# Kernel tuning notes

Hardware: AMD Instinct MI355X
Metric: run time of the kernel (lower is better)

The kernel has to match this reference:

```python
import jax, jax.numpy as jnp
import numpy as np


def setup_inputs() -> dict:
    key = jax.random.key(0)
    k1, k2, k3, k4 = jax.random.split(key, 4)
    B, n, f, k = 32768, 512, 30, 40
    X = jax.random.normal(k1, (B, n), dtype=jnp.float32)
    w1 = jax.random.normal(k2, (n, 1), dtype=jnp.float32) * 0.01
    b = jnp.zeros((1,), dtype=jnp.float32)
    v = jax.random.normal(k3, (n, f, k), dtype=jnp.float32) * 0.01
    feature2field = jax.random.randint(k4, (n,), 0, f, dtype=jnp.int32)
    return {"X": X, "w1": w1, "b": b, "v": v, "feature2field": feature2field}


def reference(X, w1, b, v, feature2field):
    # linear terms: [B]
    linear = (X @ w1).reshape(-1) + b[0]
    n = v.shape[0]
    # A[i, j] = v[i, feature2field[j]]  -> [n, n, k]
    A = v[:, feature2field, :]
    # pair coefficient C[i, j] = sum_k v[i, field[j], k] * v[j, field[i], k]
    C = jnp.einsum('ijk,jik->ij', A, A)
    # strict upper triangle matches the i<j loop in the original
    Cm = C * jnp.triu(jnp.ones((n, n), dtype=C.dtype), k=1)
    # interaction[b] = sum_{i<j} C[i,j] * X[b,i] * X[b,j]
    inter = jnp.einsum('bi,ij,bj->b', X, Cm, X)
    logits = linear + inter
    return jax.nn.sigmoid(logits)
```

## Files before the change

### kernel.cpp

```cpp
#include <hip/hip_runtime.h>
#include <hip/hip_bf16.h>
#include <math.h>


#define N_FEAT 512
#define FK 1200
#define KDIM 40
#define B_ROWS 32768
#define BM 64
#define BK 64

typedef __attribute__((ext_vector_type(8))) short short8;
typedef __attribute__((ext_vector_type(4))) float f32x4;

__device__ __forceinline__ unsigned short bf16_rne(float f) {
    union { float f; unsigned int u; } c; c.f = f;
    unsigned int u = c.u;
    u += 0x7fffu + ((u >> 16) & 1u);
    return (unsigned short)(u >> 16);
}

__device__ __forceinline__ float bf16_to_f(unsigned short h) {
    union { unsigned int u; float f; } c;
    c.u = ((unsigned int)h) << 16;
    return c.f;
}

__device__ __forceinline__ void async_copy16(const void* g, void* l) {
    __builtin_amdgcn_global_load_lds(
        (const __attribute__((address_space(1))) void*)g,
        (__attribute__((address_space(3))) void*)l,
        16, 0, 0);
}

__global__ __launch_bounds__(256) void build_w16(const float* __restrict__ v,
                                                 const int* __restrict__ f2f,
                                                 unsigned short* __restrict__ W16) {
    const int j = blockIdx.x * 256 + threadIdx.x;
    const int i = blockIdx.y;
    const int fi = f2f[i];
    const int fj = f2f[j];
    const float4* a = (const float4*)(v + (size_t)i * FK + (size_t)fj * KDIM);
    const float4* c = (const float4*)(v + (size_t)j * FK + (size_t)fi * KDIM);
    float acc = 0.f;
#pragma unroll
    for (int q = 0; q < KDIM / 4; ++q) {
        float4 av = a[q], cv = c[q];
        acc = fmaf(av.x, cv.x, acc);
        acc = fmaf(av.y, cv.y, acc);
        acc = fmaf(av.z, cv.z, acc);
        acc = fmaf(av.w, cv.w, acc);
    }
    W16[(size_t)i * N_FEAT + j] = (i == j) ? (unsigned short)0 : bf16_rne(0.5f * acc);
}

__global__ __launch_bounds__(256, 2) void ffm_fused(const float* __restrict__ X,
                                                    const unsigned short* __restrict__ W16,
                                                    const float* __restrict__ w1,
                                                    const float* __restrict__ bvec,
                                                    float* __restrict__ out) {
    __shared__ __align__(16) unsigned short As[BM * N_FEAT];
    __shared__ __align__(16) unsigned short Bs[128 * BK];
    float* part = (float*)Bs;

    const int tid  = threadIdx.x;
    const int lane = tid & 63;
    const int wave = tid >> 6;
    const int wm = wave & 1;
    const int wn = wave >> 1;
    const int quad = lane >> 4;
    const int l16  = lane & 15;

    const size_t row0 = (size_t)blockIdx.x * BM;

    {
        const float4* X4 = (const float4*)(X + row0 * N_FEAT);
        for (int u = 0; u < 16; ++u) {
            const int g  = u * 256 + tid;
            const int r  = g >> 6;
            const int cc = g & 63;
            float4 f0 = X4[r * 128 + cc * 2];
            float4 f1 = X4[r * 128 + cc * 2 + 1];
            union { unsigned short us[8]; short8 v; } pk;
            pk.us[0] = bf16_rne(f0.x);
            pk.us[1] = bf16_rne(f0.y);
            pk.us[2] = bf16_rne(f0.z);
            pk.us[3] = bf16_rne(f0.w);
            pk.us[4] = bf16_rne(f1.x);
            pk.us[5] = bf16_rne(f1.y);
            pk.us[6] = bf16_rne(f1.z);
            pk.us[7] = bf16_rne(f1.w);
            *(short8*)(As + r * N_FEAT + ((cc ^ (r & 7)) << 3)) = pk.v;
        }
    }

    const int srow = lane >> 3;
    const int scol = (((lane & 7) ^ srow) << 3);
    const int aswz = l16 & 7;

    float rs[2][4];
#pragma unroll
    for (int mi = 0; mi < 2; ++mi)
#pragma unroll
        for (int reg = 0; reg < 4; ++reg) rs[mi][reg] = 0.f;

    for (int cb = 0; cb < 4; ++cb) {
        const int col0 = cb * 128;

        f32x4 acc[2][4];
#pragma unroll
        for (int mi = 0; mi < 2; ++mi)
#pragma unroll
            for (int ni = 0; ni < 4; ++ni)
                acc[mi][ni] = (f32x4){0.f, 0.f, 0.f, 0.f};

        for (int k0 = 0; k0 < N_FEAT; k0 += BK) {
            __syncthreads();
#pragma unroll
            for (int c = 0; c < 4; ++c) {
                const int chunk = wave * 4 + c;
                const int r = chunk * 8 + srow;
                async_copy16(W16 + (size_t)(col0 + r) * N_FEAT + k0 + scol,
                             Bs + chunk * 512);
            }
            __syncthreads();

#pragma unroll
            for (int kk = 0; kk < 2; ++kk) {
                short8 a[2], b[4];
                const int kc = (k0 >> 3) + kk * 4 + quad;
#pragma unroll
                for (int mi = 0; mi < 2; ++mi) {
                    const int ar = wm * 32 + mi * 16 + l16;
                    a[mi] = *(const short8*)(As + ar * N_FEAT + ((kc ^ aswz) << 3));
                }
                const int swc = ((kk * 4 + quad) ^ aswz) << 3;
#pragma unroll
                for (int ni = 0; ni < 4; ++ni) {
                    const int br = wn * 64 + ni * 16 + l16;
                    b[ni] = *(const short8*)(Bs + br * BK + swc);
                }
#pragma unroll
                for (int mi = 0; mi < 2; ++mi)
#pragma unroll
                    for (int ni = 0; ni < 4; ++ni)
                        acc[mi][ni] = __builtin_amdgcn_mfma_f32_16x16x32_bf16(
                            a[mi], b[ni], acc[mi][ni], 0, 0, 0);
            }
        }

        float w1v[4];
#pragma unroll
        for (int ni = 0; ni < 4; ++ni)
            w1v[ni] = w1[col0 + wn * 64 + ni * 16 + l16];
#pragma unroll
        for (int mi = 0; mi < 2; ++mi) {
#pragma unroll
            for (int ni = 0; ni < 4; ++ni) {
                const int gc = col0 + wn * 64 + ni * 16 + l16;
#pragma unroll
                for (int reg = 0; reg < 4; ++reg) {
                    const int row = wm * 32 + mi * 16 + quad * 4 + reg;
                    const int adr = row * N_FEAT + ((((gc >> 3) ^ (row & 7)) << 3) | (gc & 7));
                    const float xf = bf16_to_f(As[adr]);
                    rs[mi][reg] = fmaf(xf, acc[mi][ni][reg] + w1v[ni], rs[mi][reg]);
                }
            }
        }
    }

    __syncthreads();

#pragma unroll
    for (int mi = 0; mi < 2; ++mi)
#pragma unroll
        for (int reg = 0; reg < 4; ++reg) {
            float r = rs[mi][reg];
#pragma unroll
            for (int off = 1; off < 16; off <<= 1)
                r += __shfl_xor(r, off, 16);
            if (l16 == 0)
                part[wn * BM + wm * 32 + mi * 16 + quad * 4 + reg] = r;
        }
    __syncthreads();

    if (tid < BM) {
        const float t = part[tid] + part[BM + tid] + bvec[0];
        out[row0 + tid] = 1.0f / (1.0f + expf(-t));
    }
}

extern "C" void kernel_launch(void* const* d_in, const int* in_sizes, int n_in,
                              void* d_out, int out_size, void* d_ws, size_t ws_size,
                              hipStream_t stream) {
    const float* X   = (const float*)d_in[0];
    const float* w1  = (const float*)d_in[1];
    const float* b   = (const float*)d_in[2];
    const float* v   = (const float*)d_in[3];
    const int*   f2f = (const int*)d_in[4];
    float* out = (float*)d_out;

    unsigned short* W16 = (unsigned short*)d_ws;

    build_w16<<<dim3(2, N_FEAT), 256, 0, stream>>>(v, f2f, W16);
    ffm_fused<<<B_ROWS / BM, 256, 0, stream>>>(X, W16, w1, b, out);
}
```

Before: 128.2 us.

## Load W fragments directly from global memory instead of staging through LDS

Removes the LDS staging buffer for the W16 tiles and the two barriers per K step. Each wave now loads its MFMA B fragments straight from global memory (L2-resident, 512x512 bf16) in a fully unrolled 16-step K loop. This drops synchronisation and LDS traffic. In exchange, every wave pair re-reads the same W rows from cache, and global latency is exposed with no explicit prefetch.

```diff
diff --git a/kernel.cpp b/kernel.cpp
--- a/kernel.cpp
+++ b/kernel.cpp
@@ -8,7 +8,6 @@
 #define KDIM 40
 #define B_ROWS 32768
 #define BM 64
-#define BK 64
 
 typedef __attribute__((ext_vector_type(8))) short short8;
 typedef __attribute__((ext_vector_type(4))) float f32x4;
@@ -24,13 +23,6 @@
     union { unsigned int u; float f; } c;
     c.u = ((unsigned int)h) << 16;
     return c.f;
-}
-
-__device__ __forceinline__ void async_copy16(const void* g, void* l) {
-    __builtin_amdgcn_global_load_lds(
-        (const __attribute__((address_space(1))) void*)g,
-        (__attribute__((address_space(3))) void*)l,
-        16, 0, 0);
 }
 
 __global__ __launch_bounds__(256) void build_w16(const float* __restrict__ v,
@@ -60,8 +52,7 @@
                                                     const float* __restrict__ bvec,
                                                     float* __restrict__ out) {
     __shared__ __align__(16) unsigned short As[BM * N_FEAT];
-    __shared__ __align__(16) unsigned short Bs[128 * BK];
-    float* part = (float*)Bs;
+    __shared__ float part[2 * BM];
 
     const int tid  = threadIdx.x;
     const int lane = tid & 63;
@@ -70,6 +61,7 @@
     const int wn = wave >> 1;
     const int quad = lane >> 4;
     const int l16  = lane & 15;
+    const int aswz = l16 & 7;
 
     const size_t row0 = (size_t)blockIdx.x * BM;
 
@@ -93,10 +85,7 @@
             *(short8*)(As + r * N_FEAT + ((cc ^ (r & 7)) << 3)) = pk.v;
         }
     }
-
-    const int srow = lane >> 3;
-    const int scol = (((lane & 7) ^ srow) << 3);
-    const int aswz = l16 & 7;
+    __syncthreads();
 
     float rs[2][4];
 #pragma unroll
@@ -114,39 +103,29 @@
             for (int ni = 0; ni < 4; ++ni)
                 acc[mi][ni] = (f32x4){0.f, 0.f, 0.f, 0.f};
 
-        for (int k0 = 0; k0 < N_FEAT; k0 += BK) {
-            __syncthreads();
+        const unsigned short* pb[4];
 #pragma unroll
-            for (int c = 0; c < 4; ++c) {
-                const int chunk = wave * 4 + c;
-                const int r = chunk * 8 + srow;
-                async_copy16(W16 + (size_t)(col0 + r) * N_FEAT + k0 + scol,
-                             Bs + chunk * 512);
-            }
-            __syncthreads();
+        for (int ni = 0; ni < 4; ++ni)
+            pb[ni] = W16 + (size_t)(col0 + wn * 64 + ni * 16 + l16) * N_FEAT + quad * 8;
 
 #pragma unroll
-            for (int kk = 0; kk < 2; ++kk) {
-                short8 a[2], b[4];
-                const int kc = (k0 >> 3) + kk * 4 + quad;
+        for (int kk = 0; kk < 16; ++kk) {
+            short8 a[2], b[4];
 #pragma unroll
-                for (int mi = 0; mi < 2; ++mi) {
-                    const int ar = wm * 32 + mi * 16 + l16;
-                    a[mi] = *(const short8*)(As + ar * N_FEAT + ((kc ^ aswz) << 3));
-                }
-                const int swc = ((kk * 4 + quad) ^ aswz) << 3;
+            for (int ni = 0; ni < 4; ++ni)
+                b[ni] = *(const short8*)(pb[ni] + kk * 32);
+            const int kc = kk * 4 + quad;
 #pragma unroll
-                for (int ni = 0; ni < 4; ++ni) {
-                    const int br = wn * 64 + ni * 16 + l16;
-                    b[ni] = *(const short8*)(Bs + br * BK + swc);
-                }
+            for (int mi = 0; mi < 2; ++mi) {
+                const int ar = wm * 32 + mi * 16 + l16;
+                a[mi] = *(const short8*)(As + ar * N_FEAT + ((kc ^ aswz) << 3));
+            }
 #pragma unroll
-                for (int mi = 0; mi < 2; ++mi)
+            for (int mi = 0; mi < 2; ++mi)
 #pragma unroll
-                    for (int ni = 0; ni < 4; ++ni)
-                        acc[mi][ni] = __builtin_amdgcn_mfma_f32_16x16x32_bf16(
-                            a[mi], b[ni], acc[mi][ni], 0, 0, 0);
-            }
+                for (int ni = 0; ni < 4; ++ni)
+                    acc[mi][ni] = __builtin_amdgcn_mfma_f32_16x16x32_bf16(
+                        a[mi], b[ni], acc[mi][ni], 0, 0, 0);
         }
 
         float w1v[4];
@@ -168,8 +147,6 @@
             }
         }
     }
-
-    __syncthreads();
 
 #pragma unroll
     for (int mi = 0; mi < 2; ++mi)
```

New measurement: 164.0 us. 27.9% more time.

## Double-buffer W tiles with async prefetch and use 8 waves per block

Applied to the files above, without the earlier changes.

Moves the fused FFM kernel from 256 to 512 threads, so each of 8 waves computes a 32x32 sub-tile instead of 32x64. W16 tiles are now double-buffered in LDS, and the next stage is prefetched with async global-to-LDS loads, synchronised by explicit vmcnt waits and raw barriers instead of two __syncthreads per k-step. The first W tile is issued before the X conversion, and w1 loads are hoisted out of the loop. The changes aim to hide global load latency and raise occupancy, at the cost of more LDS, more barriers per block and fragile manual waitcnt handling.

```diff
diff --git a/kernel.cpp b/kernel.cpp
--- a/kernel.cpp
+++ b/kernel.cpp
@@ -32,6 +32,8 @@
         (__attribute__((address_space(3))) void*)l,
         16, 0, 0);
 }
+
+#define FENCE() asm volatile("" ::: "memory")
 
 __global__ __launch_bounds__(256) void build_w16(const float* __restrict__ v,
                                                  const int* __restrict__ f2f,
@@ -54,14 +56,14 @@
     W16[(size_t)i * N_FEAT + j] = (i == j) ? (unsigned short)0 : bf16_rne(0.5f * acc);
 }
 
-__global__ __launch_bounds__(256, 2) void ffm_fused(const float* __restrict__ X,
+__global__ __launch_bounds__(512, 2) void ffm_fused(const float* __restrict__ X,
                                                     const unsigned short* __restrict__ W16,
                                                     const float* __restrict__ w1,
                                                     const float* __restrict__ bvec,
                                                     float* __restrict__ out) {
     __shared__ __align__(16) unsigned short As[BM * N_FEAT];
-    __shared__ __align__(16) unsigned short Bs[128 * BK];
-    float* part = (float*)Bs;
+    __shared__ __align__(16) unsigned short Bs[2][128 * BK];
+    __shared__ float part[4 * BM];
 
     const int tid  = threadIdx.x;
     const int lane = tid & 63;
@@ -70,13 +72,40 @@
     const int wn = wave >> 1;
     const int quad = lane >> 4;
     const int l16  = lane & 15;
+    const int aswz = l16 & 7;
 
     const size_t row0 = (size_t)blockIdx.x * BM;
 
+    const int srow = lane >> 3;
+    const int scol = (((lane & 7) ^ srow) << 3);
+
+    float w1v[4][2];
+#pragma unroll
+    for (int cb = 0; cb < 4; ++cb)
+#pragma unroll
+        for (int ni = 0; ni < 2; ++ni)
+            w1v[cb][ni] = w1[cb * 128 + wn * 32 + ni * 16 + l16];
+    const float bias = bvec[0];
+
+    auto stage = [&](int s) {
+        const int col0 = (s >> 3) * 128;
+        const int k0   = (s & 7) * 64;
+        unsigned short* dst = (unsigned short*)Bs[s & 1];
+#pragma unroll
+        for (int c = 0; c < 2; ++c) {
+            const int chunk = wave * 2 + c;
+            const int r = chunk * 8 + srow;
+            async_copy16(W16 + (size_t)(col0 + r) * N_FEAT + k0 + scol,
+                         dst + chunk * 512);
+        }
+    };
+
+    stage(0);
     {
         const float4* X4 = (const float4*)(X + row0 * N_FEAT);
-        for (int u = 0; u < 16; ++u) {
-            const int g  = u * 256 + tid;
+#pragma unroll
+        for (int u = 0; u < 8; ++u) {
+            const int g  = u * 512 + tid;
             const int r  = g >> 6;
             const int cc = g & 63;
             float4 f0 = X4[r * 128 + cc * 2];
@@ -93,10 +122,9 @@
             *(short8*)(As + r * N_FEAT + ((cc ^ (r & 7)) << 3)) = pk.v;
         }
     }
-
-    const int srow = lane >> 3;
-    const int scol = (((lane & 7) ^ srow) << 3);
-    const int aswz = l16 & 7;
+    asm volatile("s_waitcnt lgkmcnt(0)" ::: "memory");
+    __builtin_amdgcn_s_barrier();
+    FENCE();
 
     float rs[2][4];
 #pragma unroll
@@ -104,30 +132,33 @@
 #pragma unroll
         for (int reg = 0; reg < 4; ++reg) rs[mi][reg] = 0.f;
 
+    f32x4 acc[2][2];
+#pragma unroll
+    for (int mi = 0; mi < 2; ++mi)
+#pragma unroll
+        for (int ni = 0; ni < 2; ++ni)
+            acc[mi][ni] = (f32x4){0.f, 0.f, 0.f, 0.f};
+
+#pragma unroll
     for (int cb = 0; cb < 4; ++cb) {
         const int col0 = cb * 128;
-
-        f32x4 acc[2][4];
-#pragma unroll
-        for (int mi = 0; mi < 2; ++mi)
-#pragma unroll
-            for (int ni = 0; ni < 4; ++ni)
-                acc[mi][ni] = (f32x4){0.f, 0.f, 0.f, 0.f};
-
-        for (int k0 = 0; k0 < N_FEAT; k0 += BK) {
-            __syncthreads();
-#pragma unroll
-            for (int c = 0; c < 4; ++c) {
-                const int chunk = wave * 4 + c;
-                const int r = chunk * 8 + srow;
-                async_copy16(W16 + (size_t)(col0 + r) * N_FEAT + k0 + scol,
-                             Bs + chunk * 512);
+#pragma unroll
+        for (int t = 0; t < 8; ++t) {
+            const int s = cb * 8 + t;
+            if (s < 31) {
+                stage(s + 1);
+                asm volatile("s_waitcnt vmcnt(2)" ::: "memory");
+            } else {
+                asm volatile("s_waitcnt vmcnt(0)" ::: "memory");
             }
-            __syncthreads();
-
+            __builtin_amdgcn_s_barrier();
+            FENCE();
+
+            const unsigned short* bs = (const unsigned short*)Bs[s & 1];
+            const int k0 = t * 64;
 #pragma unroll
             for (int kk = 0; kk < 2; ++kk) {
-                short8 a[2], b[4];
+                short8 a[2], b[2];
                 const int kc = (k0 >> 3) + kk * 4 + quad;
 #pragma unroll
                 for (int mi = 0; mi < 2; ++mi) {
@@ -136,40 +167,39 @@
                 }
                 const int swc = ((kk * 4 + quad) ^ aswz) << 3;
 #pragma unroll
-                for (int ni = 0; ni < 4; ++ni) {
-                    const int br = wn * 64 + ni * 16 + l16;
-                    b[ni] = *(const short8*)(Bs + br * BK + swc);
+                for (int ni = 0; ni < 2; ++ni) {
+                    const int br = wn * 32 + ni * 16 + l16;
+                    b[ni] = *(const short8*)(bs + br * BK + swc);
                 }
 #pragma unroll
                 for (int mi = 0; mi < 2; ++mi)
 #pragma unroll
-                    for (int ni = 0; ni < 4; ++ni)
+                    for (int ni = 0; ni < 2; ++ni)
                         acc[mi][ni] = __builtin_amdgcn_mfma_f32_16x16x32_bf16(
                             a[mi], b[ni], acc[mi][ni], 0, 0, 0);
             }
-        }
-
-        float w1v[4];
-#pragma unroll
-        for (int ni = 0; ni < 4; ++ni)
-            w1v[ni] = w1[col0 + wn * 64 + ni * 16 + l16];
+
+            FENCE();
+            __builtin_amdgcn_s_barrier();
+            FENCE();
+        }
+
 #pragma unroll
         for (int mi = 0; mi < 2; ++mi) {
 #pragma unroll
-            for (int ni = 0; ni < 4; ++ni) {
-                const int gc = col0 + wn * 64 + ni * 16 + l16;
+            for (int ni = 0; ni < 2; ++ni) {
+                const int gc = col0 + wn * 32 + ni * 16 + l16;
 #pragma unroll
                 for (int reg = 0; reg < 4; ++reg) {
                     const int row = wm * 32 + mi * 16 + quad * 4 + reg;
                     const int adr = row * N_FEAT + ((((gc >> 3) ^ (row & 7)) << 3) | (gc & 7));
                     const float xf = bf16_to_f(As[adr]);
-                    rs[mi][reg] = fmaf(xf, acc[mi][ni][reg] + w1v[ni], rs[mi][reg]);
+                    rs[mi][reg] = fmaf(xf, acc[mi][ni][reg] + w1v[cb][ni], rs[mi][reg]);
                 }
+                acc[mi][ni] = (f32x4){0.f, 0.f, 0.f, 0.f};
             }
         }
     }
-
-    __syncthreads();
 
 #pragma unroll
     for (int mi = 0; mi < 2; ++mi)
@@ -185,7 +215,8 @@
     __syncthreads();
 
     if (tid < BM) {
-        const float t = part[tid] + part[BM + tid] + bvec[0];
+        const float t = part[tid] + part[BM + tid] + part[2 * BM + tid] +
+                        part[3 * BM + tid] + bias;
         out[row0 + tid] = 1.0f / (1.0f + expf(-t));
     }
 }
@@ -203,5 +234,5 @@
     unsigned short* W16 = (unsigned short*)d_ws;
 
     build_w16<<<dim3(2, N_FEAT), 256, 0, stream>>>(v, f2f, W16);
-    ffm_fused<<<B_ROWS / BM, 256, 0, stream>>>(X, W16, w1, b, out);
-}
+    ffm_fused<<<B_ROWS / BM, 512, 0, stream>>>(X, W16, w1, b, out);
+}
```

Measured after the change: 141.7 us. 1.11x slower.
